# Optimization experiments

Hardware: AMD Instinct MI355X
Metric: run time of the kernel (lower is better)

The kernel has to match this reference:

```python
import jax, jax.numpy as jnp
import numpy as np

B, S, D, H = 2, 2048, 2048, 16
HD = D // H  # 128


def setup_inputs() -> dict:
    key = jax.random.key(0)
    ks = jax.random.split(key, 7)
    x = jax.random.normal(ks[0], (B, S, D), jnp.float32)
    # 4 tree-position components per token (e.g. depth/branch coordinates)
    pos = jax.random.uniform(ks[1], (B, S, 4), jnp.float32, 0.0, 64.0)
    # tree/causal additive mask: 0 where attending is allowed, -1e9 otherwise
    causal = jnp.where(jnp.tril(jnp.ones((S, S), bool)), 0.0, -1e9).astype(jnp.float32)
    mask = jnp.broadcast_to(causal, (B, S, S))
    scale = D ** -0.5
    wq = jax.random.normal(ks[2], (D, D), jnp.float32) * scale
    wk = jax.random.normal(ks[3], (D, D), jnp.float32) * scale
    wv = jax.random.normal(ks[4], (D, D), jnp.float32) * scale
    wo = jax.random.normal(ks[5], (D, D), jnp.float32) * scale
    return {"x": x, "pos": pos, "mask": mask, "wq": wq, "wk": wk, "wv": wv, "wo": wo}


def reference(x, pos, mask, wq, wk, wv, wo):
    b, s, d = x.shape
    hd = HD
    # theta_of_dims: 1/10000^(arange(0,hd,8)[:hd//8]/hd) -> [hd//8]
    theta = 1.0 / (10000.0 ** (jnp.arange(0, hd, 8)[: hd // 8].astype(jnp.float32) / hd))
    q = (x @ wq.T).reshape(b, s, H, hd)
    k = (x @ wk.T).reshape(b, s, H, hd)
    v = (x @ wv.T).reshape(b, s, H, hd)
    # freqs: [b, s, hd//8, 4] flattened to [b, s, 1, hd//2]
    freqs = jnp.einsum('bij,k->bikj', pos, theta).reshape(b, s, 1, hd // 2)
    cos, sin = jnp.cos(freqs), jnp.sin(freqs)

    def rope(t):
        tr, ti = t[..., 0::2], t[..., 1::2]  # complex pairs (even=real, odd=imag)
        out_r = tr * cos - ti * sin
        out_i = tr * sin + ti * cos
        return jnp.stack([out_r, out_i], axis=-1).reshape(t.shape)

    q, k = rope(q), rope(k)
    scores = jnp.einsum('bqhd,bkhd->bhqk', q, k) / np.float32(np.sqrt(hd))
    scores = scores + mask[:, None, :, :]
    attn = jax.nn.softmax(scores, axis=-1)
    out = jnp.einsum('bhqk,bkhd->bqhd', attn, v).reshape(b, s, d)
    return out @ wo.T
```

## Files before the change

### kernel.cpp

```cpp
#include <hip/hip_runtime.h>
#include <cstdint>
#include <type_traits>

typedef __attribute__((ext_vector_type(8))) short short8;
typedef __attribute__((ext_vector_type(4))) float floatx4;

#define NB 2
#define NS 2048
#define ND 2048
#define NH 16
#define NHD 128

__device__ __forceinline__ float b2f(short s) {
  unsigned u = ((unsigned)(unsigned short)s) << 16;
  return __builtin_bit_cast(float, u);
}
__device__ __forceinline__ short f2b(float f) {
  unsigned u = __builtin_bit_cast(unsigned, f);
  unsigned r = (u + 0x7fffu + ((u >> 16) & 1u)) >> 16;
  return (short)(unsigned short)r;
}

__global__ void cast_all(const float* __restrict__ x, const float* __restrict__ wq,
                         const float* __restrict__ wk, const float* __restrict__ wv,
                         const float* __restrict__ wo, short* __restrict__ dst) {
  const int i = blockIdx.x * blockDim.x + threadIdx.x;
  const float* src;
  int off;
  if (i < 2097152) { src = x;  off = i; }
  else if (i < 3145728) { src = wq; off = i - 2097152; }
  else if (i < 4194304) { src = wk; off = i - 3145728; }
  else if (i < 5242880) { src = wv; off = i - 4194304; }
  else { src = wo; off = i - 5242880; }
  float4 v = ((const float4*)src)[off];
  short4 o;
  o.x = f2b(v.x); o.y = f2b(v.y); o.z = f2b(v.z); o.w = f2b(v.w);
  ((short4*)dst)[i] = o;
}

__device__ __forceinline__ void gld_lds16(const void* g, void* l) {
  __builtin_amdgcn_global_load_lds((const __attribute__((address_space(1))) void*)g,
                                   (__attribute__((address_space(3))) void*)l,
                                   16, 0, 0);
}

__global__ __launch_bounds__(256) void qkv_gemm(const short* __restrict__ A,
                                                const short* __restrict__ Bt,
                                                short* __restrict__ Qh,
                                                short* __restrict__ Kh,
                                                short* __restrict__ vlin) {
  constexpr int K = 2048;
  __shared__ short As[128 * 64];
  __shared__ short Bs[128 * 64];
  const int m0 = blockIdx.y * 128, n0 = blockIdx.x * 128;
  const int which = n0 >> 11;
  const int nl0 = n0 & 2047;
  const int t = threadIdx.x;
  const int wave = t >> 6, lane = t & 63, l15 = lane & 15, quad = lane >> 4;
  const int wm = (wave >> 1) * 64, wn = (wave & 1) * 64;

  floatx4 acc[4][4] = {};

  const int srow = t >> 3;
  const int scol = (t & 7) ^ (srow & 7);
  const short* Ag = A + (long)(m0 + srow) * K + scol * 8;
  const short* Bg = Bt + (long)(n0 + srow) * K + scol * 8;
  char* AsB = (char*)As;
  char* BsB = (char*)Bs;
  const int ldsOff = wave * 1024;

  for (int kt = 0; kt < K; kt += 64) {
#pragma unroll
    for (int i = 0; i < 4; ++i) {
      gld_lds16(Ag + kt + (long)(32 * i) * K, AsB + ldsOff + i * 4096);
      gld_lds16(Bg + kt + (long)(32 * i) * K, BsB + ldsOff + i * 4096);
    }
    __syncthreads();

#pragma unroll
    for (int half = 0; half < 2; ++half) {
      short8 a[4], b[4];
#pragma unroll
      for (int mi = 0; mi < 4; ++mi) {
        const int rr = wm + mi * 16 + l15;
        a[mi] = *(const short8*)&As[rr * 64 + (((half << 2) | quad) ^ (rr & 7)) * 8];
      }
#pragma unroll
      for (int ni = 0; ni < 4; ++ni) {
        const int rr = wn + ni * 16 + l15;
        b[ni] = *(const short8*)&Bs[rr * 64 + (((half << 2) | quad) ^ (rr & 7)) * 8];
      }
#pragma unroll
      for (int mi = 0; mi < 4; ++mi)
#pragma unroll
        for (int ni = 0; ni < 4; ++ni)
          acc[mi][ni] = __builtin_amdgcn_mfma_f32_16x16x32_bf16(a[mi], b[ni], acc[mi][ni], 0, 0, 0);
    }
    __syncthreads();
  }

  short* headDst = (which == 0) ? Qh : Kh;
#pragma unroll
  for (int mi = 0; mi < 4; ++mi) {
#pragma unroll
    for (int ni = 0; ni < 4; ++ni) {
#pragma unroll
      for (int r = 0; r < 4; ++r) {
        const int row = m0 + wm + mi * 16 + quad * 4 + r;
        const int col = nl0 + wn + ni * 16 + l15;
        const short v = f2b(acc[mi][ni][r]);
        if (which == 2) {
          vlin[(long)row * 2048 + col] = v;
        } else {
          const int bb = row >> 11, s = row & 2047, h = col >> 7, hd = col & 127;
          headDst[(((long)(bb * 16 + h) * 2048) + s) * 128 + hd] = v;
        }
      }
    }
  }
}

__global__ __launch_bounds__(256) void gemm_out(const short* __restrict__ A,
                                                const short* __restrict__ Bt,
                                                float* __restrict__ Cout) {
  constexpr int K = 2048, N = 2048;
  __shared__ short As[128 * 64];
  __shared__ short Bs[128 * 64];
  const int m0 = blockIdx.y * 128, n0 = blockIdx.x * 128;
  const int t = threadIdx.x;
  const int wave = t >> 6, lane = t & 63, l15 = lane & 15, quad = lane >> 4;
  const int wm = (wave >> 1) * 64, wn = (wave & 1) * 64;

  floatx4 acc[4][4] = {};

  const int srow = t >> 3;
  const int scol = (t & 7) ^ (srow & 7);
  const short* Ag = A + (long)(m0 + srow) * K + scol * 8;
  const short* Bg = Bt + (long)(n0 + srow) * K + scol * 8;
  char* AsB = (char*)As;
  char* BsB = (char*)Bs;
  const int ldsOff = wave * 1024;

  for (int kt = 0; kt < K; kt += 64) {
#pragma unroll
    for (int i = 0; i < 4; ++i) {
      gld_lds16(Ag + kt + (long)(32 * i) * K, AsB + ldsOff + i * 4096);
      gld_lds16(Bg + kt + (long)(32 * i) * K, BsB + ldsOff + i * 4096);
    }
    __syncthreads();

#pragma unroll
    for (int half = 0; half < 2; ++half) {
      short8 a[4], b[4];
#pragma unroll
      for (int mi = 0; mi < 4; ++mi) {
        const int rr = wm + mi * 16 + l15;
        a[mi] = *(const short8*)&As[rr * 64 + (((half << 2) | quad) ^ (rr & 7)) * 8];
      }
#pragma unroll
      for (int ni = 0; ni < 4; ++ni) {
        const int rr = wn + ni * 16 + l15;
        b[ni] = *(const short8*)&Bs[rr * 64 + (((half << 2) | quad) ^ (rr & 7)) * 8];
      }
#pragma unroll
      for (int mi = 0; mi < 4; ++mi)
#pragma unroll
        for (int ni = 0; ni < 4; ++ni)
          acc[mi][ni] = __builtin_amdgcn_mfma_f32_16x16x32_bf16(a[mi], b[ni], acc[mi][ni], 0, 0, 0);
    }
    __syncthreads();
  }

#pragma unroll
  for (int mi = 0; mi < 4; ++mi)
#pragma unroll
    for (int ni = 0; ni < 4; ++ni)
#pragma unroll
      for (int r = 0; r < 4; ++r) {
        const int row = m0 + wm + mi * 16 + quad * 4 + r;
        const int col = n0 + wn + ni * 16 + l15;
        Cout[(long)row * N + col] = acc[mi][ni][r];
      }
}

__global__ __launch_bounds__(256) void rope_vtrans(short* __restrict__ Qh,
                                                   short* __restrict__ Kh,
                                                   const float* __restrict__ pos,
                                                   const short* __restrict__ v_lin,
                                                   short* __restrict__ Vt) {
  __shared__ short tile[64 * 72];
  const int bx = blockIdx.x;
  if (bx < 4096) {
    const int tid = bx * 256 + threadIdx.x;
    const int kk = tid & 15;
    const int h = (tid >> 4) & 15;
    const int token = tid >> 8;
    const int bb = token >> 11, s = token & 2047;
    const float4 p4 = ((const float4*)pos)[token];
    const float pv[4] = {p4.x, p4.y, p4.z, p4.w};
    const float theta = exp2f(-(float)kk * 0.8304820237218406f);
    const long base = (((long)(bb * 16 + h)) * 2048 + s) * 128 + kk * 8;
    short8 q8 = *(short8*)(Qh + base);
    short8 k8 = *(short8*)(Kh + base);
    short8 qo, ko;
#pragma unroll
    for (int jj = 0; jj < 4; ++jj) {
      const float fr = pv[jj] * theta;
      float sn, c;
      __sincosf(fr, &sn, &c);
      {
        const float tr = b2f(q8[2 * jj]), ti = b2f(q8[2 * jj + 1]);
        qo[2 * jj] = f2b(tr * c - ti * sn);
        qo[2 * jj + 1] = f2b(tr * sn + ti * c);
      }
      {
        const float tr = b2f(k8[2 * jj]), ti = b2f(k8[2 * jj + 1]);
        ko[2 * jj] = f2b(tr * c - ti * sn);
        ko[2 * jj + 1] = f2b(tr * sn + ti * c);
      }
    }
    *(short8*)(Qh + base) = qo;
    *(short8*)(Kh + base) = ko;
  } else {
    const int b2 = bx - 4096;
    const int s0 = (b2 & 31) * 64;
    const int hd0 = ((b2 >> 5) & 1) * 64;
    const int bh = b2 >> 6;
    const int bb = bh >> 4, h = bh & 15;
    const int t = threadIdx.x;
#pragma unroll
    for (int i = 0; i < 2; ++i) {
      const int ch = t + i * 256;
      const int r = ch >> 3, c = ch & 7;
      *(short8*)&tile[r * 72 + c * 8] =
          *(const short8*)(v_lin + (long)(bb * 2048 + s0 + r) * 2048 + h * 128 + hd0 + c * 8);
    }
    __syncthreads();
#pragma unroll
    for (int i = 0; i < 2; ++i) {
      const int ch = t + i * 256;
      const int r2 = ch >> 3, c2 = ch & 7;
      short8 o;
#pragma unroll
      for (int u = 0; u < 8; ++u) o[u] = tile[(c2 * 8 + u) * 72 + r2];
      *(short8*)(Vt + ((long)(bh * 128 + hd0 + r2)) * 2048 + s0 + c2 * 8) = o;
    }
  }
}

__global__ __launch_bounds__(256, 3) void flash(const short* __restrict__ Qh,
                                                const short* __restrict__ Kh,
                                                const short* __restrict__ Vt,
                                                short* __restrict__ ao) {
  __shared__ short Ks[64 * 128];
  __shared__ short Vts[128 * 64];
  __shared__ short Ps[4 * 16 * 64];
  const int id = blockIdx.x;
  const int qt = 31 - (id >> 5);
  const int bh = id & 31;
  const int t = threadIdx.x, wave = t >> 6, lane = t & 63, l15 = lane & 15, quad = lane >> 4;
  const int sqb = qt * 64;
  const int lastkt = qt;

  const short* Qbase = Qh + (long)bh * 2048 * 128;
  short8 aq[4];
#pragma unroll
  for (int ks = 0; ks < 4; ++ks)
    aq[ks] = *(const short8*)(Qbase + (long)(sqb + wave * 16 + l15) * 128 + ks * 32 + quad * 8);

  const short* KgBase = Kh + (long)bh * 2048 * 128;
  const short* VgBase = Vt + (long)bh * 128 * 2048;

  short8 kreg[4], vreg[4];
#pragma unroll
  for (int i = 0; i < 4; ++i) {
    const int ch = t + i * 256;
    kreg[i] = *(const short8*)(KgBase + (long)(ch >> 4) * 128 + (ch & 15) * 8);
    vreg[i] = *(const short8*)(VgBase + (long)(ch >> 3) * 2048 + (ch & 7) * 8);
  }

  float l_part[4] = {};
  floatx4 acc_o[8] = {};
  const float CEXP = 0.12751745f;

  for (int kt = 0; kt <= lastkt; ++kt) {
    const int k0 = kt * 64;
    if (kt > 0) __syncthreads();

#pragma unroll
    for (int i = 0; i < 4; ++i) {
      const int ch = t + i * 256;
      const int kr = ch >> 4, kc = ch & 15;
      *(short8*)&Ks[kr * 128 + (((kc & 7) ^ (kr & 7)) | (kc & 8)) * 8] = kreg[i];
      const int vr = ch >> 3, vc = ch & 7;
      *(short8*)&Vts[vr * 64 + (vc ^ (vr & 7)) * 8] = vreg[i];
    }
    __syncthreads();

    if (kt < lastkt) {
      const short* Kg = KgBase + (long)(k0 + 64) * 128;
      const short* Vg = VgBase + (k0 + 64);
#pragma unroll
      for (int i = 0; i < 4; ++i) {
        const int ch = t + i * 256;
        kreg[i] = *(const short8*)(Kg + (long)(ch >> 4) * 128 + (ch & 15) * 8);
        vreg[i] = *(const short8*)(Vg + (long)(ch >> 3) * 2048 + (ch & 7) * 8);
      }
    }

    const bool dg = (kt == lastkt);
    floatx4 accs[4] = {};
    __builtin_amdgcn_s_setprio(1);
#pragma unroll
    for (int ks = 0; ks < 4; ++ks) {
#pragma unroll
      for (int ni = 0; ni < 4; ++ni) {
        const int rr = ni * 16 + l15;
        const int c = ks * 4 + quad;
        const short8 bk = *(const short8*)&Ks[rr * 128 + (((c & 7) ^ (rr & 7)) | (c & 8)) * 8];
        accs[ni] = __builtin_amdgcn_mfma_f32_16x16x32_bf16(aq[ks], bk, accs[ni], 0, 0, 0);
      }
    }
    __builtin_amdgcn_s_setprio(0);
#pragma unroll
    for (int r = 0; r < 4; ++r) {
      const int qrow = sqb + wave * 16 + quad * 4 + r;
      const int prow = quad * 4 + r;
#pragma unroll
      for (int ni = 0; ni < 4; ++ni) {
        float e = exp2f(accs[ni][r] * CEXP);
        if (dg && (k0 + ni * 16 + l15) > qrow) e = 0.f;
        const int pc = ni * 2 + (l15 >> 3);
        Ps[wave * 1024 + prow * 64 + (pc ^ (prow & 7)) * 8 + (l15 & 7)] = f2b(e);
        l_part[r] += e;
      }
    }
    __builtin_amdgcn_s_setprio(1);
#pragma unroll
    for (int ks2 = 0; ks2 < 2; ++ks2) {
      const int pc = ks2 * 4 + quad;
      const short8 ap = *(const short8*)&Ps[wave * 1024 + l15 * 64 + (pc ^ (l15 & 7)) * 8];
#pragma unroll
      for (int nh = 0; nh < 8; ++nh) {
        const int vr = nh * 16 + l15;
        const short8 bv = *(const short8*)&Vts[vr * 64 + (pc ^ (vr & 7)) * 8];
        acc_o[nh] = __builtin_amdgcn_mfma_f32_16x16x32_bf16(ap, bv, acc_o[nh], 0, 0, 0);
      }
    }
    __builtin_amdgcn_s_setprio(0);
  }

  const int bb = bh >> 4, h = bh & 15;
#pragma unroll
  for (int r = 0; r < 4; ++r) {
    float rs = l_part[r];
#pragma unroll
    for (int mm = 8; mm >= 1; mm >>= 1) rs += __shfl_xor(rs, mm, 16);
    const float inv = 1.0f / rs;
    const int s = sqb + wave * 16 + quad * 4 + r;
    const long rowbase = ((long)(bb * 2048 + s)) * 2048 + h * 128;
#pragma unroll
    for (int nh = 0; nh < 8; ++nh) ao[rowbase + nh * 16 + l15] = f2b(acc_o[nh][r] * inv);
  }
}

extern "C" void kernel_launch(void* const* d_in, const int* in_sizes, int n_in,
                              void* d_out, int out_size, void* d_ws, size_t ws_size,
                              hipStream_t stream) {
  const float* x = (const float*)d_in[0];
  const float* pos = (const float*)d_in[1];
  const float* wq = (const float*)d_in[3];
  const float* wk = (const float*)d_in[4];
  const float* wv = (const float*)d_in[5];
  const float* wo = (const float*)d_in[6];
  float* out = (float*)d_out;

  char* ws = (char*)d_ws;
  const size_t MB = 1024 * 1024;
  short* xb    = (short*)(ws + 0);
  short* wqkvb = (short*)(ws + 16 * MB);
  short* wob   = (short*)(ws + 40 * MB);
  short* Qh    = (short*)(ws + 48 * MB);
  short* Kh    = (short*)(ws + 64 * MB);
  short* Vt    = (short*)(ws + 80 * MB);
  short* vlin  = (short*)(ws + 96 * MB);
  short* ao    = (short*)(ws + 96 * MB);

  cast_all<<<24576, 256, 0, stream>>>(x, wq, wk, wv, wo, xb);

  qkv_gemm<<<dim3(48, 32), 256, 0, stream>>>(xb, wqkvb, Qh, Kh, vlin);

  rope_vtrans<<<6144, 256, 0, stream>>>(Qh, Kh, pos, vlin, Vt);

  flash<<<1024, 256, 0, stream>>>(Qh, Kh, Vt, ao);

  gemm_out<<<dim3(16, 32), 256, 0, stream>>>(ao, wob, out);
}
```

Baseline: 391.9 us.

## Pipeline QKV GEMM with triple-buffered LDS and 256x128 tiles

Rewrites the QKV projection GEMM to use 512-thread blocks computing 256x128 tiles, with a three-stage LDS ring buffer filled by async global-to-LDS loads issued two k-steps ahead. Each k-tile is split into two halves, and the prefetch loads are interleaved with the LDS fragment reads. Explicit vmcnt waits, barriers and s_setprio raise MFMA priority. The goal is to hide global-load latency behind compute and raise reuse of each B tile, at the cost of 144KB of LDS per block, which limits occupancy to one block per CU, plus tighter manual synchronisation.

```diff
diff --git a/kernel.cpp b/kernel.cpp
--- a/kernel.cpp
+++ b/kernel.cpp
@@ -44,20 +44,19 @@
                                    16, 0, 0);
 }
 
-__global__ __launch_bounds__(256) void qkv_gemm(const short* __restrict__ A,
-                                                const short* __restrict__ Bt,
-                                                short* __restrict__ Qh,
-                                                short* __restrict__ Kh,
-                                                short* __restrict__ vlin) {
-  constexpr int K = 2048;
-  __shared__ short As[128 * 64];
-  __shared__ short Bs[128 * 64];
-  const int m0 = blockIdx.y * 128, n0 = blockIdx.x * 128;
+__global__ __launch_bounds__(512, 2) void qkv_gemm(const short* __restrict__ A,
+                                                   const short* __restrict__ Bt,
+                                                   short* __restrict__ Qh,
+                                                   short* __restrict__ Kh,
+                                                   short* __restrict__ vlin) {
+  constexpr int K = 2048, NT = K / 64;
+  __shared__ __align__(16) char lds[147456];
+  const int m0 = blockIdx.y * 256, n0 = blockIdx.x * 128;
   const int which = n0 >> 11;
   const int nl0 = n0 & 2047;
   const int t = threadIdx.x;
   const int wave = t >> 6, lane = t & 63, l15 = lane & 15, quad = lane >> 4;
-  const int wm = (wave >> 1) * 64, wn = (wave & 1) * 64;
+  const int wr = wave >> 1, wc = wave & 1;
 
   floatx4 acc[4][4] = {};
 
@@ -65,38 +64,88 @@
   const int scol = (t & 7) ^ (srow & 7);
   const short* Ag = A + (long)(m0 + srow) * K + scol * 8;
   const short* Bg = Bt + (long)(n0 + srow) * K + scol * 8;
-  char* AsB = (char*)As;
-  char* BsB = (char*)Bs;
-  const int ldsOff = wave * 1024;
-
-  for (int kt = 0; kt < K; kt += 64) {
-#pragma unroll
-    for (int i = 0; i < 4; ++i) {
-      gld_lds16(Ag + kt + (long)(32 * i) * K, AsB + ldsOff + i * 4096);
-      gld_lds16(Bg + kt + (long)(32 * i) * K, BsB + ldsOff + i * 4096);
-    }
-    __syncthreads();
-
-#pragma unroll
-    for (int half = 0; half < 2; ++half) {
+  const int wOff = wave * 1024;
+
+#pragma unroll
+  for (int i = 0; i < 4; ++i) gld_lds16(Ag + (long)(i * 64) * K, lds + 0 * 32768 + i * 8192 + wOff);
+#pragma unroll
+  for (int i = 0; i < 2; ++i) gld_lds16(Bg + (long)(i * 64) * K, lds + 98304 + 0 * 16384 + i * 8192 + wOff);
+#pragma unroll
+  for (int i = 0; i < 4; ++i) gld_lds16(Ag + 64 + (long)(i * 64) * K, lds + 1 * 32768 + i * 8192 + wOff);
+#pragma unroll
+  for (int i = 0; i < 2; ++i) gld_lds16(Bg + 64 + (long)(i * 64) * K, lds + 98304 + 1 * 16384 + i * 8192 + wOff);
+  asm volatile("s_waitcnt vmcnt(6)" ::: "memory");
+  __builtin_amdgcn_s_barrier();
+
+  int scur = 0;
+  for (int T = 0; T < NT; ++T) {
+    const int snext = (scur >= 1) ? scur - 1 : scur + 2;
+    const short* At = (const short*)(lds + scur * 32768);
+    const short* Btl = (const short*)(lds + 98304 + scur * 16384);
+    char* An = lds + snext * 32768;
+    char* Bn = lds + 98304 + snext * 16384;
+    const long knext = (long)(T + 2) * 64;
+    const bool more = (T + 2) < NT;
+
+    {
       short8 a[4], b[4];
 #pragma unroll
       for (int mi = 0; mi < 4; ++mi) {
-        const int rr = wm + mi * 16 + l15;
-        a[mi] = *(const short8*)&As[rr * 64 + (((half << 2) | quad) ^ (rr & 7)) * 8];
+        const int rr = wr * 64 + mi * 16 + l15;
+        a[mi] = *(const short8*)&At[rr * 64 + (quad ^ (rr & 7)) * 8];
       }
 #pragma unroll
       for (int ni = 0; ni < 4; ++ni) {
-        const int rr = wn + ni * 16 + l15;
-        b[ni] = *(const short8*)&Bs[rr * 64 + (((half << 2) | quad) ^ (rr & 7)) * 8];
-      }
+        const int rr = wc * 64 + ni * 16 + l15;
+        b[ni] = *(const short8*)&Btl[rr * 64 + (quad ^ (rr & 7)) * 8];
+      }
+      if (more) {
+#pragma unroll
+        for (int i = 0; i < 3; ++i) gld_lds16(Ag + knext + (long)(i * 64) * K, An + i * 8192 + wOff);
+      }
+      __builtin_amdgcn_s_barrier();
+      __builtin_amdgcn_s_setprio(1);
 #pragma unroll
       for (int mi = 0; mi < 4; ++mi)
 #pragma unroll
         for (int ni = 0; ni < 4; ++ni)
           acc[mi][ni] = __builtin_amdgcn_mfma_f32_16x16x32_bf16(a[mi], b[ni], acc[mi][ni], 0, 0, 0);
-    }
-    __syncthreads();
+      __builtin_amdgcn_s_setprio(0);
+      __builtin_amdgcn_s_barrier();
+    }
+
+    {
+      short8 a[4], b[4];
+#pragma unroll
+      for (int mi = 0; mi < 4; ++mi) {
+        const int rr = wr * 64 + mi * 16 + l15;
+        a[mi] = *(const short8*)&At[rr * 64 + ((4 | quad) ^ (rr & 7)) * 8];
+      }
+#pragma unroll
+      for (int ni = 0; ni < 4; ++ni) {
+        const int rr = wc * 64 + ni * 16 + l15;
+        b[ni] = *(const short8*)&Btl[rr * 64 + ((4 | quad) ^ (rr & 7)) * 8];
+      }
+      if (more) {
+        gld_lds16(Ag + knext + (long)(3 * 64) * K, An + 3 * 8192 + wOff);
+#pragma unroll
+        for (int i = 0; i < 2; ++i) gld_lds16(Bg + knext + (long)(i * 64) * K, Bn + i * 8192 + wOff);
+        asm volatile("s_waitcnt vmcnt(6)" ::: "memory");
+      } else {
+        asm volatile("s_waitcnt vmcnt(0)" ::: "memory");
+      }
+      __builtin_amdgcn_s_barrier();
+      __builtin_amdgcn_s_setprio(1);
+#pragma unroll
+      for (int mi = 0; mi < 4; ++mi)
+#pragma unroll
+        for (int ni = 0; ni < 4; ++ni)
+          acc[mi][ni] = __builtin_amdgcn_mfma_f32_16x16x32_bf16(a[mi], b[ni], acc[mi][ni], 0, 0, 0);
+      __builtin_amdgcn_s_setprio(0);
+      __builtin_amdgcn_s_barrier();
+    }
+
+    scur = (scur + 1 == 3) ? 0 : scur + 1;
   }
 
   short* headDst = (which == 0) ? Qh : Kh;
@@ -106,8 +155,8 @@
     for (int ni = 0; ni < 4; ++ni) {
 #pragma unroll
       for (int r = 0; r < 4; ++r) {
-        const int row = m0 + wm + mi * 16 + quad * 4 + r;
-        const int col = nl0 + wn + ni * 16 + l15;
+        const int row = m0 + wr * 64 + mi * 16 + quad * 4 + r;
+        const int col = nl0 + wc * 64 + ni * 16 + l15;
         const short v = f2b(acc[mi][ni][r]);
         if (which == 2) {
           vlin[(long)row * 2048 + col] = v;
@@ -388,7 +437,7 @@
 
   cast_all<<<24576, 256, 0, stream>>>(x, wq, wk, wv, wo, xb);
 
-  qkv_gemm<<<dim3(48, 32), 256, 0, stream>>>(xb, wqkvb, Qh, Kh, vlin);
+  qkv_gemm<<<dim3(48, 16), 512, 0, stream>>>(xb, wqkvb, Qh, Kh, vlin);
 
   rope_vtrans<<<6144, 256, 0, stream>>>(Qh, Kh, pos, vlin, Vt);
 
```

Measured after the change: 389.7 us. Within noise of the previous version (-0.5%).
